# Performance work log

Measured on AMD Instinct MI355X. Metric: run time of the kernel, lower is better.

Reference implementation:

```python
import jax, jax.numpy as jnp
import numpy as np

D_MODEL = 2048
HQ = 32
HKV = 8
DK = D_MODEL // HQ  # 64
GROUP = HQ // HKV   # 4


def setup_inputs() -> dict:
    key = jax.random.key(0)
    ks = jax.random.split(key, 9)
    B, S = 2, 2048
    scale = 0.02
    x = jax.random.normal(ks[0], (B, S, D_MODEL), dtype=jnp.float32)
    W_q = jax.random.normal(ks[1], (D_MODEL, D_MODEL), dtype=jnp.float32) * scale
    b_q = jnp.zeros((D_MODEL,), dtype=jnp.float32)
    W_k = jax.random.normal(ks[2], (D_MODEL, HKV * DK), dtype=jnp.float32) * scale
    b_k = jnp.zeros((HKV * DK,), dtype=jnp.float32)
    W_v = jax.random.normal(ks[3], (D_MODEL, HKV * DK), dtype=jnp.float32) * scale
    b_v = jnp.zeros((HKV * DK,), dtype=jnp.float32)
    W_o = jax.random.normal(ks[4], (D_MODEL, D_MODEL), dtype=jnp.float32) * scale
    b_o = jnp.zeros((D_MODEL,), dtype=jnp.float32)
    return {"x": x, "W_q": W_q, "b_q": b_q, "W_k": W_k, "b_k": b_k,
            "W_v": W_v, "b_v": b_v, "W_o": W_o, "b_o": b_o}


def reference(x, W_q, b_q, W_k, b_k, W_v, b_v, W_o, b_o):
    B, S, _ = x.shape
    # Projections -> [B, H, S, d_k]
    Q = (x @ W_q + b_q).reshape(B, S, HQ, DK).transpose(0, 2, 1, 3)
    K = (x @ W_k + b_k).reshape(B, S, HKV, DK).transpose(0, 2, 1, 3)
    V = (x @ W_v + b_v).reshape(B, S, HKV, DK).transpose(0, 2, 1, 3)
    # repeat_interleave over head dim to match query heads
    K = jnp.repeat(K, GROUP, axis=1)  # [B, HQ, S, DK]
    V = jnp.repeat(V, GROUP, axis=1)
    scores = jnp.einsum('bhqd,bhkd->bhqk', Q, K) / jnp.sqrt(jnp.float32(DK))
    attn = jax.nn.softmax(scores, axis=-1)
    out = jnp.einsum('bhqk,bhkd->bhqd', attn, V)  # [B, HQ, S, DK]
    out = out.transpose(0, 2, 1, 3).reshape(B, S, HQ * DK)
    return out @ W_o + b_o
```

## Files before the change

### kernel.cpp

```cpp
#include <hip/hip_runtime.h>
#include <stdint.h>

#define S_LEN 2048
#define NTOK  4096
#define DMODEL 2048
#define NHQ 32
#define NHKV 8

typedef _Float16 half8 __attribute__((ext_vector_type(8)));
typedef _Float16 half4v __attribute__((ext_vector_type(4)));
typedef __fp16 fp16x2 __attribute__((ext_vector_type(2)));
typedef float f32x4 __attribute__((ext_vector_type(4)));
typedef float f32x16 __attribute__((ext_vector_type(16)));

#define MFMA16(a,b,c) __builtin_amdgcn_mfma_f32_16x16x32_f16(a,b,c,0,0,0)
#define MFMA32(a,b,c) __builtin_amdgcn_mfma_f32_32x32x16_f16(a,b,c,0,0,0)

__device__ __forceinline__ void gload16(const void* g, void* l) {
  __builtin_amdgcn_global_load_lds(
      (const __attribute__((address_space(1))) void*)g,
      (__attribute__((address_space(3))) void*)l, 16, 0, 0);
}

__device__ __forceinline__ float fexp2(float x) {
#if __has_builtin(__builtin_amdgcn_exp2f)
  return __builtin_amdgcn_exp2f(x);
#else
  float r; asm("v_exp_f32 %0, %1" : "=v"(r) : "v"(x)); return r;
#endif
}

__device__ __forceinline__ int cvt_pk(float a, float b) {
  fp16x2 r = __builtin_amdgcn_cvt_pkrtz(a, b);
  return __builtin_bit_cast(int, r);
}


__global__ void cast_x(const float* __restrict__ x, _Float16* __restrict__ xs) {
  size_t i = ((size_t)blockIdx.x * 256 + threadIdx.x) * 4;
  float4 v = *(const float4*)(x + i);
  half4v o = {(_Float16)v.x, (_Float16)v.y, (_Float16)v.z, (_Float16)v.w};
  *(half4v*)(xs + i) = o;
}

__global__ void prep_w(const float* __restrict__ W, _Float16* __restrict__ Wt,
                       int K, int N) {
  __shared__ float tile[32][33];
  int kt = blockIdx.x * 32, nt = blockIdx.y * 32;
  int r = threadIdx.x >> 5, c = threadIdx.x & 31;
#pragma unroll
  for (int i = 0; i < 4; i++)
    tile[r + i * 8][c] = W[(size_t)(kt + r + i * 8) * N + nt + c];
  __syncthreads();
#pragma unroll
  for (int i = 0; i < 4; i++) {
    int rr = r + i * 8;
    Wt[(size_t)(nt + rr) * K + kt + c] = (_Float16)tile[c][rr];
  }
}

template<int MODE>
__global__ __launch_bounds__(256) void gemm_nt(
    const _Float16* __restrict__ A, const _Float16* __restrict__ Bt, int K,
    const float* __restrict__ bias1, const float* __restrict__ bias2,
    const float* __restrict__ bias3,
    _Float16* __restrict__ outQ, _Float16* __restrict__ outK,
    _Float16* __restrict__ outV, float* __restrict__ outF)
{
  __shared__ __align__(16) _Float16 As[2][128 * 32];
  __shared__ __align__(16) _Float16 Bs[2][128 * 32];
  const int tid = threadIdx.x;
  const int w = tid >> 6, l = tid & 63;
  const int wr = w >> 1, wc = w & 1;

  const int lin = blockIdx.x + blockIdx.y * 32;
  const int nwg = gridDim.x * gridDim.y;
  const int swz = (lin & 7) * (nwg >> 3) + (lin >> 3);
  const int row0 = (swz & 31) * 128, col0 = (swz >> 5) * 128;

  f32x4 acc[4][4] = {};

  const int lr = l >> 2;
  const int scol = 8 * ((l & 3) ^ (lr & 3));
  const _Float16* Abase = A + (size_t)row0 * K;
  const _Float16* Bbase = Bt + (size_t)col0 * K;

  const int fr = l & 15;
  const int rswz = 8 * ((l >> 4) ^ (l & 3));

#define GSTAGE(buf, kt)                                                       \
  {                                                                           \
    _Pragma("unroll")                                                         \
    for (int s = 0; s < 2; s++) {                                             \
      int r = s * 64 + w * 16 + lr;                                           \
      gload16(Abase + (size_t)r * K + (kt) * 32 + scol,                       \
              &As[buf][(s * 64 + w * 16) * 32]);                              \
      gload16(Bbase + (size_t)r * K + (kt) * 32 + scol,                       \
              &Bs[buf][(s * 64 + w * 16) * 32]);                              \
    }                                                                         \
  }

  const int NK = K >> 5;
  GSTAGE(0, 0);
  __syncthreads();

  for (int kt = 0; kt < NK; kt++) {
    const int cur = kt & 1;
    if (kt + 1 < NK) GSTAGE(cur ^ 1, kt + 1);

    half8 af[4], bf[4];
#pragma unroll
    for (int m = 0; m < 4; m++)
      af[m] = *(const half8*)&As[cur][(wr * 64 + m * 16 + fr) * 32 + rswz];
#pragma unroll
    for (int n = 0; n < 4; n++)
      bf[n] = *(const half8*)&Bs[cur][(wc * 64 + n * 16 + fr) * 32 + rswz];
    __builtin_amdgcn_s_setprio(1);
#pragma unroll
    for (int m = 0; m < 4; m++)
#pragma unroll
      for (int n = 0; n < 4; n++)
        acc[m][n] = MFMA16(af[m], bf[n], acc[m][n]);
    __builtin_amdgcn_s_setprio(0);

    __syncthreads();
  }
#undef GSTAGE

  const int rl = (l >> 4) * 4;
  const int cl = l & 15;
#pragma unroll
  for (int m = 0; m < 4; m++) {
#pragma unroll
    for (int n = 0; n < 4; n++) {
#pragma unroll
      for (int j = 0; j < 4; j++) {
        int grow = row0 + wr * 64 + m * 16 + rl + j;
        int gcol = col0 + wc * 64 + n * 16 + cl;
        float v = acc[m][n][j];
        if (MODE == 0) {
          int b = grow >> 11, s = grow & 2047;
          if (gcol < 2048) {
            float v2 = (v + bias1[gcol]) * 0.1803368801111137f;
            int h = gcol >> 6, d = gcol & 63;
            outQ[((size_t)((b * NHQ + h) * S_LEN + s)) * 64 + d] = (_Float16)v2;
          } else if (gcol < 2560) {
            int kc = gcol - 2048;
            float v2 = v + bias2[kc];
            int h = kc >> 6, d = kc & 63;
            outK[((size_t)((b * NHKV + h) * S_LEN + s)) * 64 + d] = (_Float16)v2;
          } else {
            int vc = gcol - 2560;
            float v2 = v + bias3[vc];
            int h = vc >> 6, d = vc & 63;
            int sl = s & 63;
            int pos = (sl & 51) | ((sl & 4) << 1) | ((sl & 8) >> 1);
            int col = (s & ~63) | (pos ^ ((d & 7) * 8));
            outV[((size_t)((b * NHKV + h) * 64 + d)) * 2048 + col] = (_Float16)v2;
          }
        } else {
          float v2 = v + bias1[gcol];
          outF[(size_t)grow * DMODEL + gcol] = v2;
        }
      }
    }
  }
}

__global__ __launch_bounds__(256, 3) void fa_kernel(
    const _Float16* __restrict__ Qs, const _Float16* __restrict__ Ks,
    const _Float16* __restrict__ Vt, _Float16* __restrict__ Ao)
{
  __shared__ __align__(16) _Float16 Kls[2][64 * 64];
  __shared__ __align__(16) _Float16 Vls[2][64 * 64];
  const int tid = threadIdx.x;
  const int w = tid >> 6, l = tid & 63;
  const int q0 = blockIdx.x * 128;
  const int bh = blockIdx.y;
  const int b = bh >> 5, hh = bh & 31, hk = hh >> 2;

  const _Float16* Qg = Qs + ((size_t)(b * NHQ + hh) * S_LEN) * 64;
  const _Float16* Kg = Ks + ((size_t)(b * NHKV + hk) * S_LEN) * 64;
  const _Float16* Vg = Vt + ((size_t)(b * NHKV + hk) * 64) * 2048;

  const int lq = l & 31;
  const int hf = l >> 5;
  const int lx7 = lq & 7;

  half8 qf[4];
  {
    const _Float16* qrow = Qg + (size_t)(q0 + w * 32 + lq) * 64 + hf * 8;
#pragma unroll
    for (int dc = 0; dc < 4; dc++)
      qf[dc] = *(const half8*)&qrow[dc * 16];
  }

  half8 ones;
#pragma unroll
  for (int i = 0; i < 8; i++) ones[i] = (_Float16)1.0f;

  const int sr0 = w * 16 + (l >> 3);
  const _Float16* kp = Kg + (size_t)sr0 * 64 + 8 * ((l & 7) ^ (sr0 & 7));
  const _Float16* vp = Vg + (size_t)sr0 * 2048 + 8 * (l & 7);

  f32x16 acc0 = {}, acc1 = {}, accl = {};

#define STAGE(buf, t)                                                         \
  {                                                                           \
    _Pragma("unroll")                                                         \
    for (int i = 0; i < 2; i++) {                                             \
      gload16(kp + (size_t)((t) * 64 + i * 8) * 64,                           \
              &Kls[buf][(w * 16 + i * 8) * 64]);                              \
      gload16(vp + (size_t)(t) * 64 + (size_t)(i * 8) * 2048,                 \
              &Vls[buf][(w * 16 + i * 8) * 64]);                              \
    }                                                                         \
  }

  STAGE(0, 0);
  __syncthreads();

  const int NT = S_LEN / 64;
  int cur = 0;
  for (int t = 0; t < NT; t++) {
    if (t + 1 < NT) STAGE(cur ^ 1, t + 1);

    f32x16 s0 = {}, s1 = {};
    __builtin_amdgcn_s_setprio(1);
#pragma unroll
    for (int dc = 0; dc < 4; dc++) {
      int oct = ((dc * 2 + hf) ^ lx7) * 8;
      half8 kf0 = *(const half8*)&Kls[cur][lq * 64 + oct];
      half8 kf1 = *(const half8*)&Kls[cur][(32 + lq) * 64 + oct];
      s0 = MFMA32(kf0, qf[dc], s0);
      s1 = MFMA32(kf1, qf[dc], s1);
    }
    __builtin_amdgcn_s_setprio(0);

    half8 pf[4];
#define PACKC(c, SA)                                                          \
    {                                                                         \
      int4 pi;                                                                \
      pi.x = cvt_pk(fexp2(SA[8 * ((c) & 1) + 0]), fexp2(SA[8 * ((c) & 1) + 1])); \
      pi.y = cvt_pk(fexp2(SA[8 * ((c) & 1) + 2]), fexp2(SA[8 * ((c) & 1) + 3])); \
      pi.z = cvt_pk(fexp2(SA[8 * ((c) & 1) + 4]), fexp2(SA[8 * ((c) & 1) + 5])); \
      pi.w = cvt_pk(fexp2(SA[8 * ((c) & 1) + 6]), fexp2(SA[8 * ((c) & 1) + 7])); \
      pf[c] = __builtin_bit_cast(half8, pi);                                  \
    }
    PACKC(0, s0) PACKC(1, s0) PACKC(2, s1) PACKC(3, s1)
#undef PACKC

    __builtin_amdgcn_s_setprio(1);
#pragma unroll
    for (int c = 0; c < 4; c++) {
      int oct = ((c * 2 + hf) ^ lx7) * 8;
      half8 vf0 = *(const half8*)&Vls[cur][lq * 64 + oct];
      half8 vf1 = *(const half8*)&Vls[cur][(32 + lq) * 64 + oct];
      acc0 = MFMA32(vf0, pf[c], acc0);
      acc1 = MFMA32(vf1, pf[c], acc1);
      accl = MFMA32(ones, pf[c], accl);
    }
    __builtin_amdgcn_s_setprio(0);

    __syncthreads();
    cur ^= 1;
  }

  const float inv = 1.0f / accl[0];
  _Float16* abase = Ao + ((size_t)(b * S_LEN + q0 + w * 32 + lq)) * DMODEL + hh * 64;
#pragma unroll
  for (int dt = 0; dt < 2; dt++) {
#pragma unroll
    for (int mreg = 0; mreg < 4; mreg++) {
      half4v hv;
#pragma unroll
      for (int j = 0; j < 4; j++) {
        float v = (dt == 0 ? acc0[mreg * 4 + j] : acc1[mreg * 4 + j]) * inv;
        hv[j] = (_Float16)v;
      }
      *(half4v*)&abase[dt * 32 + mreg * 8 + hf * 4] = hv;
    }
  }
#undef STAGE
}

extern "C" void kernel_launch(void* const* d_in, const int* in_sizes, int n_in,
                              void* d_out, int out_size, void* d_ws, size_t ws_size,
                              hipStream_t stream) {
  const float* x   = (const float*)d_in[0];
  const float* W_q = (const float*)d_in[1];
  const float* b_q = (const float*)d_in[2];
  const float* W_k = (const float*)d_in[3];
  const float* b_k = (const float*)d_in[4];
  const float* W_v = (const float*)d_in[5];
  const float* b_v = (const float*)d_in[6];
  const float* W_o = (const float*)d_in[7];
  const float* b_o = (const float*)d_in[8];

  char* ws = (char*)d_ws;
  _Float16* xs    = (_Float16*)(ws);
  _Float16* Wall  = (_Float16*)(ws + (16ull << 20));
  _Float16* Wo_t  = (_Float16*)(ws + (28ull << 20));
  _Float16* Qsb   = (_Float16*)(ws + (36ull << 20));
  _Float16* Ksb   = (_Float16*)(ws + (68ull << 20));
  _Float16* Vtb   = (_Float16*)(ws + (80ull << 20));
  _Float16* Ao    = (_Float16*)(ws + (88ull << 20));

  cast_x<<<8192, 256, 0, stream>>>(x, xs);
  prep_w<<<dim3(64, 64), 256, 0, stream>>>(W_q, Wall, 2048, 2048);
  prep_w<<<dim3(64, 16), 256, 0, stream>>>(W_k, Wall + (size_t)2048 * 2048, 2048, 512);
  prep_w<<<dim3(64, 16), 256, 0, stream>>>(W_v, Wall + (size_t)2560 * 2048, 2048, 512);
  prep_w<<<dim3(64, 64), 256, 0, stream>>>(W_o, Wo_t, 2048, 2048);

  gemm_nt<0><<<dim3(32, 24), 256, 0, stream>>>(xs, Wall, 2048, b_q, b_k, b_v,
                                               Qsb, Ksb, Vtb, nullptr);
  fa_kernel<<<dim3(16, 64), 256, 0, stream>>>(Qsb, Ksb, Vtb, Ao);
  gemm_nt<2><<<dim3(32, 16), 256, 0, stream>>>(Ao, Wo_t, 2048, b_o, nullptr, nullptr,
                                               nullptr, nullptr, nullptr, (float*)d_out);
}
```

Measured before the change: 244.7 us.

## Replace GEMM with 256x256-tile 8-wave kernel using phased interleaved prefetch

The 128x128 tile GEMM with 4 waves is replaced by a 256x256 tile, 512-thread kernel with a 64-wide K step. Global-to-LDS loads are split into eight phases and interleaved with MFMA bursts, using explicit vmcnt waits and raw barriers. The aim is more data reuse per LDS byte and better overlap of memory traffic with compute. The cost is only 192 and 128 workgroups for the two GEMMs, which may underfill the 256 CUs, plus 128KB of LDS per block.

```diff
diff --git a/kernel.cpp b/kernel.cpp
--- a/kernel.cpp
+++ b/kernel.cpp
@@ -60,83 +60,110 @@
 }
 
 template<int MODE>
-__global__ __launch_bounds__(256) void gemm_nt(
+__global__ __launch_bounds__(512, 1) void gemm8(
     const _Float16* __restrict__ A, const _Float16* __restrict__ Bt, int K,
     const float* __restrict__ bias1, const float* __restrict__ bias2,
     const float* __restrict__ bias3,
     _Float16* __restrict__ outQ, _Float16* __restrict__ outK,
     _Float16* __restrict__ outV, float* __restrict__ outF)
 {
-  __shared__ __align__(16) _Float16 As[2][128 * 32];
-  __shared__ __align__(16) _Float16 Bs[2][128 * 32];
+  __shared__ __align__(16) _Float16 Als[2][256 * 64];
+  __shared__ __align__(16) _Float16 Bls[2][256 * 64];
   const int tid = threadIdx.x;
   const int w = tid >> 6, l = tid & 63;
-  const int wr = w >> 1, wc = w & 1;
-
-  const int lin = blockIdx.x + blockIdx.y * 32;
-  const int nwg = gridDim.x * gridDim.y;
+  const int wr = w >> 2, wc = w & 3;
+
+  const int lin = blockIdx.x + blockIdx.y * 16;
+  const int nwg = 16 * gridDim.y;
   const int swz = (lin & 7) * (nwg >> 3) + (lin >> 3);
-  const int row0 = (swz & 31) * 128, col0 = (swz >> 5) * 128;
-
-  f32x4 acc[4][4] = {};
-
-  const int lr = l >> 2;
-  const int scol = 8 * ((l & 3) ^ (lr & 3));
-  const _Float16* Abase = A + (size_t)row0 * K;
-  const _Float16* Bbase = Bt + (size_t)col0 * K;
-
-  const int fr = l & 15;
-  const int rswz = 8 * ((l >> 4) ^ (l & 3));
-
-#define GSTAGE(buf, kt)                                                       \
+  const int row0 = (swz & 15) * 256, col0 = (swz >> 4) * 256;
+
+  const int g0 = l >> 4, fr = l & 15, fx = fr & 7;
+  const int sl = l & 7, sr = l >> 3;
+
+  const _Float16* Ab = A + (size_t)row0 * K + 8 * (sl ^ sr);
+  const _Float16* Bb = Bt + (size_t)col0 * K + 8 * (sl ^ sr);
+
+  f32x4 acc[8][4] = {};
+  half8 bf[4][2];
+
+#define STG(GB, LS, buf, h, kt)                                               \
+  { _Pragma("unroll")                                                         \
+    for (int i = 0; i < 2; i++)                                               \
+      gload16(GB + (size_t)((h) * 128 + i * 64 + w * 8 + sr) * K + (kt) * 64, \
+              &LS[buf][((h) * 128 + i * 64 + w * 8) * 64]); }
+
+#define RDA(buf, m, s) \
+  (*(const half8*)&Als[buf][(wr * 128 + (m) * 16 + fr) * 64 + 8 * ((((s) * 4 + g0)) ^ fx)])
+#define RDB(buf, n, s) \
+  (*(const half8*)&Bls[buf][(wc * 64 + (n) * 16 + fr) * 64 + 8 * ((((s) * 4 + g0)) ^ fx)])
+
+#define PHASE(buf, p, STAGES, WAITC)                                          \
   {                                                                           \
+    if ((p) == 0) {                                                           \
+      _Pragma("unroll")                                                       \
+      for (int n = 0; n < 4; n++) {                                           \
+        bf[n][0] = RDB(buf, n, 0);                                            \
+        bf[n][1] = RDB(buf, n, 1);                                            \
+      }                                                                       \
+    }                                                                         \
+    half8 a00 = RDA(buf, 2 * (p), 0), a01 = RDA(buf, 2 * (p), 1);             \
+    half8 a10 = RDA(buf, 2 * (p) + 1, 0), a11 = RDA(buf, 2 * (p) + 1, 1);     \
+    STAGES;                                                                   \
+    WAITC;                                                                    \
+    __builtin_amdgcn_s_barrier();                                             \
+    asm volatile("s_waitcnt lgkmcnt(0)" ::: "memory");                        \
+    __builtin_amdgcn_sched_barrier(0);                                        \
+    __builtin_amdgcn_s_setprio(1);                                            \
     _Pragma("unroll")                                                         \
-    for (int s = 0; s < 2; s++) {                                             \
-      int r = s * 64 + w * 16 + lr;                                           \
-      gload16(Abase + (size_t)r * K + (kt) * 32 + scol,                       \
-              &As[buf][(s * 64 + w * 16) * 32]);                              \
-      gload16(Bbase + (size_t)r * K + (kt) * 32 + scol,                       \
-              &Bs[buf][(s * 64 + w * 16) * 32]);                              \
+    for (int n = 0; n < 4; n++) {                                             \
+      acc[2 * (p)][n]     = MFMA16(a00, bf[n][0], acc[2 * (p)][n]);           \
+      acc[2 * (p)][n]     = MFMA16(a01, bf[n][1], acc[2 * (p)][n]);           \
+      acc[2 * (p) + 1][n] = MFMA16(a10, bf[n][0], acc[2 * (p) + 1][n]);       \
+      acc[2 * (p) + 1][n] = MFMA16(a11, bf[n][1], acc[2 * (p) + 1][n]);       \
     }                                                                         \
-  }
-
-  const int NK = K >> 5;
-  GSTAGE(0, 0);
-  __syncthreads();
-
-  for (int kt = 0; kt < NK; kt++) {
-    const int cur = kt & 1;
-    if (kt + 1 < NK) GSTAGE(cur ^ 1, kt + 1);
-
-    half8 af[4], bf[4];
-#pragma unroll
-    for (int m = 0; m < 4; m++)
-      af[m] = *(const half8*)&As[cur][(wr * 64 + m * 16 + fr) * 32 + rswz];
-#pragma unroll
-    for (int n = 0; n < 4; n++)
-      bf[n] = *(const half8*)&Bs[cur][(wc * 64 + n * 16 + fr) * 32 + rswz];
-    __builtin_amdgcn_s_setprio(1);
-#pragma unroll
-    for (int m = 0; m < 4; m++)
-#pragma unroll
-      for (int n = 0; n < 4; n++)
-        acc[m][n] = MFMA16(af[m], bf[n], acc[m][n]);
-    __builtin_amdgcn_s_setprio(0);
-
-    __syncthreads();
-  }
-#undef GSTAGE
-
-  const int rl = (l >> 4) * 4;
-  const int cl = l & 15;
-#pragma unroll
-  for (int m = 0; m < 4; m++) {
+    __builtin_amdgcn_s_setprio(0);                                            \
+    __builtin_amdgcn_s_barrier();                                             \
+  }
+
+  const int NKT = K >> 6;
+  const int NIT = NKT >> 1;
+
+  STG(Ab, Als, 0, 0, 0) STG(Ab, Als, 0, 1, 0)
+  STG(Bb, Bls, 0, 0, 0) STG(Bb, Bls, 0, 1, 0)
+  STG(Bb, Bls, 1, 0, 1) STG(Bb, Bls, 1, 1, 1)
+  asm volatile("s_waitcnt vmcnt(4)" ::: "memory");
+  __builtin_amdgcn_s_barrier();
+
+  for (int it = 0; it < NIT; it++) {
+    const int t0 = 2 * it, t1 = t0 + 1;
+    const bool more = (it + 1 < NIT);
+    PHASE(0, 0, { STG(Ab, Als, 1, 0, t1) STG(Ab, Als, 1, 1, t1) }, )
+    PHASE(0, 1, { if (more) STG(Bb, Bls, 0, 0, t0 + 2) }, )
+    PHASE(0, 2, { if (more) STG(Bb, Bls, 0, 1, t0 + 2) }, )
+    PHASE(0, 3, ,
+          if (more) { asm volatile("s_waitcnt vmcnt(4)" ::: "memory"); }
+          else      { asm volatile("s_waitcnt vmcnt(0)" ::: "memory"); } )
+    PHASE(1, 0, { if (more) STG(Ab, Als, 0, 0, t0 + 2) }, )
+    PHASE(1, 1, { if (more) STG(Ab, Als, 0, 1, t0 + 2) }, )
+    PHASE(1, 2, { if (more) STG(Bb, Bls, 1, 0, t1 + 2) }, )
+    PHASE(1, 3, { if (more) STG(Bb, Bls, 1, 1, t1 + 2) },
+          if (more) { asm volatile("s_waitcnt vmcnt(4)" ::: "memory"); } )
+  }
+#undef PHASE
+#undef RDA
+#undef RDB
+#undef STG
+
+  const int rl = g0 * 4;
+#pragma unroll
+  for (int m = 0; m < 8; m++) {
 #pragma unroll
     for (int n = 0; n < 4; n++) {
 #pragma unroll
       for (int j = 0; j < 4; j++) {
-        int grow = row0 + wr * 64 + m * 16 + rl + j;
-        int gcol = col0 + wc * 64 + n * 16 + cl;
+        int grow = row0 + wr * 128 + m * 16 + rl + j;
+        int gcol = col0 + wc * 64 + n * 16 + fr;
         float v = acc[m][n][j];
         if (MODE == 0) {
           int b = grow >> 11, s = grow & 2047;
@@ -153,8 +180,8 @@
             int vc = gcol - 2560;
             float v2 = v + bias3[vc];
             int h = vc >> 6, d = vc & 63;
-            int sl = s & 63;
-            int pos = (sl & 51) | ((sl & 4) << 1) | ((sl & 8) >> 1);
+            int slq = s & 63;
+            int pos = (slq & 51) | ((slq & 4) << 1) | ((slq & 8) >> 1);
             int col = (s & ~63) | (pos ^ ((d & 7) * 8));
             outV[((size_t)((b * NHKV + h) * 64 + d)) * 2048 + col] = (_Float16)v2;
           }
@@ -311,9 +338,9 @@
   prep_w<<<dim3(64, 16), 256, 0, stream>>>(W_v, Wall + (size_t)2560 * 2048, 2048, 512);
   prep_w<<<dim3(64, 64), 256, 0, stream>>>(W_o, Wo_t, 2048, 2048);
 
-  gemm_nt<0><<<dim3(32, 24), 256, 0, stream>>>(xs, Wall, 2048, b_q, b_k, b_v,
-                                               Qsb, Ksb, Vtb, nullptr);
+  gemm8<0><<<dim3(16, 12), 512, 0, stream>>>(xs, Wall, 2048, b_q, b_k, b_v,
+                                             Qsb, Ksb, Vtb, nullptr);
   fa_kernel<<<dim3(16, 64), 256, 0, stream>>>(Qsb, Ksb, Vtb, Ao);
-  gemm_nt<2><<<dim3(32, 16), 256, 0, stream>>>(Ao, Wo_t, 2048, b_o, nullptr, nullptr,
-                                               nullptr, nullptr, nullptr, (float*)d_out);
-}
+  gemm8<2><<<dim3(16, 8), 512, 0, stream>>>(Ao, Wo_t, 2048, b_o, nullptr, nullptr,
+                                            nullptr, nullptr, nullptr, (float*)d_out);
+}
```

Measured after the change: 259.0 us. +5.9%, slower.
